# Optimization experiments

Hardware: AMD Instinct MI355X
Metric: run time of the kernel (lower is better)

Reference implementation:

```python
import jax, jax.numpy as jnp
import numpy as np
import math

FRACTION = 1.0 / math.e  # GOLDEN_ZONE_CENTER


def setup_inputs() -> dict:
    key = jax.random.key(0)
    x = jax.random.normal(key, (4, 4096, 2048), dtype=jnp.float32)
    return {"x": x}


def reference(x) -> jnp.ndarray:
    # Training-mode forward of BoltzmannGateSTE: keep only top-k (k = n/e)
    # activations by global magnitude, zero the rest.
    flat = jnp.abs(x).reshape(-1)
    n = flat.shape[0]
    k = max(1, int(n * FRACTION))  # static python int -> jit-friendly
    if k >= n:
        return x
    topk_vals, _ = jax.lax.top_k(flat, k)
    threshold = topk_vals[-1]  # k-th largest magnitude
    mask = (jnp.abs(x) >= threshold).astype(x.dtype)
    return x * mask
```

## Files before the change

### kernel.cpp

```cpp
#include <hip/hip_runtime.h>
#include <stdint.h>
#include <string.h>


#define SEL_T 1024

constexpr unsigned LO_BITS = 0x3F6147AEu;
constexpr unsigned HI_BITS = 0x3F6B851Fu;
constexpr unsigned NKEY    = HI_BITS - LO_BITS;
constexpr int      NCB     = (NKEY + 1023) / 1024;

constexpr int P_GRID = 4096;
constexpr int P_BLK  = 256;
constexpr int P_WPB  = P_BLK / 64;
constexpr int NWAVES = P_GRID * P_WPB;
constexpr int CAPW   = 128;

constexpr int NBIN1   = 4096;
constexpr int NFINE   = 1 << 19;
constexpr int NCOARSE = 512;
constexpr int F_GRID  = 256;
constexpr int F_BLK   = 256;

#define S_PREF 0
#define S_K1   1
#define S_T    2
#define S_FLAG 3

__device__ __forceinline__ bool gate_skip(const unsigned* state, int gate) {
    if (gate == 0) return false;
    unsigned fl = state[S_FLAG];
    return (gate == 1) ? (fl == 0u) : (fl != 0u);
}

__global__ __launch_bounds__(P_BLK, 8)
void pass_partition(const uint4* __restrict__ x, long long n4,
                    uint4* __restrict__ out, uint2* __restrict__ cand,
                    unsigned* __restrict__ wavecnt, unsigned* __restrict__ blkchi,
                    unsigned* __restrict__ fineH, unsigned* __restrict__ state)
{
    typedef unsigned uv4 __attribute__((ext_vector_type(4)));
    const int lane  = threadIdx.x & 63;
    const int wid   = threadIdx.x >> 6;
    const int gwave = blockIdx.x * P_WPB + wid;
    uint2* my = cand + (size_t)gwave * CAPW;
    const unsigned long long lt = (1ull << lane) - 1ull;

    unsigned wcnt = 0;
    unsigned chi  = 0;
    const long long stride = (long long)gridDim.x * P_BLK;
#pragma unroll 2
    for (long long i = (long long)blockIdx.x * P_BLK + threadIdx.x; i < n4; i += stride) {
        uint4 v = x[i];
        uint4 r;
        unsigned idx0 = (unsigned)(i << 2);
#define DO_COMP(c, off)                                                        \
        { unsigned b = v.c, u = b & 0x7FFFFFFFu;                               \
          bool kp = (u >= HI_BITS);                                            \
          bool cd = (u >= LO_BITS) & !kp;                                      \
          chi += (unsigned)kp;                                                 \
          r.c = kp ? b : 0u;                                                   \
          unsigned long long m = __ballot(cd);                                 \
          if (cd) {                                                            \
              atomicAdd(&fineH[u - LO_BITS], 1u);         \
              unsigned pos = wcnt + (unsigned)__popcll(m & lt);                \
              if (pos < (unsigned)CAPW) my[pos] = make_uint2(b, idx0 + off);   \
          }                                                                    \
          wcnt += (unsigned)__popcll(m); }
        DO_COMP(x, 0) DO_COMP(y, 1) DO_COMP(z, 2) DO_COMP(w, 3)
#undef DO_COMP
        __builtin_nontemporal_store(*(uv4*)&r, (uv4*)(out + i));
    }

    for (int m = 32; m; m >>= 1) chi += __shfl_xor(chi, m, 64);
    __shared__ unsigned s_chi[P_WPB];
    if (lane == 0) {
        s_chi[wid] = chi;
        wavecnt[gwave] = (wcnt < (unsigned)CAPW) ? wcnt : (unsigned)CAPW;
        if (wcnt > (unsigned)CAPW) atomicOr(&state[S_FLAG], 1u);
    }
    __syncthreads();
    if (threadIdx.x == 0) {
        unsigned a = 0;
        for (int w = 0; w < P_WPB; ++w) a += s_chi[w];
        blkchi[blockIdx.x] = a;
    }
}

__global__ __launch_bounds__(64)
void coarse_reduce(const unsigned* __restrict__ fineH, unsigned* __restrict__ coarseH)
{
    unsigned base = blockIdx.x << 10;
    unsigned s = 0;
    for (int t = threadIdx.x; t < 1024; t += 64) {
        unsigned key = base + t;
        s += (key < NKEY) ? fineH[key] : 0u;
    }
    for (int m = 32; m; m >>= 1) s += __shfl_xor(s, m, 64);
    if (threadIdx.x == 0) coarseH[blockIdx.x] = s;
}

__device__ void select_desc(const unsigned* __restrict__ hist, int nbins,
                            unsigned k, unsigned* s_scan, int* s_res)
{
    int tid = threadIdx.x;
    if (tid == 0) { s_res[0] = -1; s_res[1] = 0; }
    __syncthreads();
    unsigned running = 0;
    for (int top = nbins; top > 0; top -= SEL_T) {
        int bin = top - 1 - tid;
        unsigned v = (bin >= 0) ? hist[bin] : 0u;
        s_scan[tid] = v;
        __syncthreads();
        for (int off = 1; off < SEL_T; off <<= 1) {
            unsigned add = (tid >= off) ? s_scan[tid - off] : 0u;
            __syncthreads();
            s_scan[tid] += add;
            __syncthreads();
        }
        unsigned p     = s_scan[tid];
        unsigned pprev = (tid > 0) ? s_scan[tid - 1] : 0u;
        unsigned total = s_scan[SEL_T - 1];
        __syncthreads();
        if (running + total >= k) {
            if (bin >= 0 && running + p >= k && running + pprev < k) {
                s_res[0] = bin;
                s_res[1] = (int)(k - running - pprev);
            }
            __syncthreads();
            return;
        }
        running += total;
    }
    __syncthreads();
}

__global__ __launch_bounds__(SEL_T)
void fast_select(const unsigned* __restrict__ blkchi, const unsigned* __restrict__ wavecnt,
                 const unsigned* __restrict__ coarseH, const unsigned* __restrict__ fineH,
                 unsigned* __restrict__ state, unsigned k)
{
    if (state[S_FLAG]) return;
    __shared__ unsigned s_scan[SEL_T];
    __shared__ int s_res[2];
    __shared__ unsigned long long s_red[SEL_T / 64][2];
    __shared__ unsigned s_kp;
    __shared__ int s_bad;

    unsigned long long chi = 0, tot = 0;
    for (int i = threadIdx.x; i < P_GRID; i += SEL_T) chi += blkchi[i];
    for (int i = threadIdx.x; i < NWAVES; i += SEL_T) tot += wavecnt[i];
    for (int m = 32; m; m >>= 1) {
        chi += __shfl_xor(chi, m, 64);
        tot += __shfl_xor(tot, m, 64);
    }
    int wid = threadIdx.x >> 6, lane = threadIdx.x & 63;
    if (lane == 0) { s_red[wid][0] = chi; s_red[wid][1] = tot; }
    __syncthreads();
    if (threadIdx.x == 0) {
        unsigned long long C = 0, Tt = 0;
        for (int w = 0; w < SEL_T / 64; ++w) { C += s_red[w][0]; Tt += s_red[w][1]; }
        if (C >= (unsigned long long)k || C + Tt < (unsigned long long)k) {
            state[S_FLAG] = 1u;
            s_bad = 1;
        } else { s_bad = 0; s_kp = (unsigned)((unsigned long long)k - C); }
    }
    __syncthreads();
    if (s_bad) return;
    unsigned kp = s_kp;

    select_desc(coarseH, NCB, kp, s_scan, s_res);
    int cb      = s_res[0];
    unsigned r  = (unsigned)s_res[1];
    __syncthreads();
    int nfine = (int)NKEY - cb * 1024;
    if (nfine > 1024) nfine = 1024;
    select_desc(fineH + (size_t)cb * 1024, nfine, r, s_scan, s_res);
    int f = s_res[0];
    if (threadIdx.x == 0)
        state[S_T] = LO_BITS + (unsigned)(cb * 1024 + f);
}

__global__ __launch_bounds__(256)
void cand_fixup(const uint2* __restrict__ cand, const unsigned* __restrict__ state,
                float* __restrict__ out, long long n)
{
    if (state[S_FLAG]) return;
    unsigned T = state[S_T];
    long long total = (long long)NWAVES * CAPW;
    long long stride = (long long)gridDim.x * 256;
    for (long long j = (long long)blockIdx.x * 256 + threadIdx.x; j < total; j += stride) {
        uint2 e = cand[j];
        if ((e.x & 0x7FFFFFFFu) >= T && e.y < (unsigned long long)n)
            out[e.y] = __uint_as_float(e.x);
    }
}

__global__ __launch_bounds__(F_BLK)
void f_hist1(const uint4* __restrict__ x, long long n4, unsigned* __restrict__ histA,
             const unsigned* __restrict__ state, int gate)
{
    if (gate_skip(state, gate)) return;
    __shared__ unsigned h[NBIN1];
    for (int i = threadIdx.x; i < NBIN1; i += F_BLK) h[i] = 0u;
    __syncthreads();
    long long stride = (long long)gridDim.x * F_BLK;
    for (long long i = (long long)blockIdx.x * F_BLK + threadIdx.x; i < n4; i += stride) {
        uint4 v = x[i];
        atomicAdd(&h[(v.x & 0x7FFFFFFFu) >> 19], 1u);
        atomicAdd(&h[(v.y & 0x7FFFFFFFu) >> 19], 1u);
        atomicAdd(&h[(v.z & 0x7FFFFFFFu) >> 19], 1u);
        atomicAdd(&h[(v.w & 0x7FFFFFFFu) >> 19], 1u);
    }
    __syncthreads();
    for (int i = threadIdx.x; i < NBIN1; i += F_BLK)
        if (h[i]) atomicAdd(&histA[i], h[i]);
}

__global__ __launch_bounds__(SEL_T)
void f_select1(const unsigned* __restrict__ histA, unsigned* __restrict__ state,
               unsigned k, int gate)
{
    if (gate_skip(state, gate)) return;
    __shared__ unsigned s_scan[SEL_T];
    __shared__ int s_res[2];
    select_desc(histA, NBIN1, k, s_scan, s_res);
    if (threadIdx.x == 0) {
        state[S_PREF] = (s_res[0] < 0) ? 0u : (unsigned)s_res[0];
        state[S_K1]   = (s_res[0] < 0) ? 1u : (unsigned)s_res[1];
    }
}

__global__ __launch_bounds__(F_BLK)
void f_hist2(const uint4* __restrict__ x, long long n4, const unsigned* __restrict__ state,
             unsigned* __restrict__ fineB, unsigned* __restrict__ coarseB, int gate)
{
    if (gate_skip(state, gate)) return;
    __shared__ unsigned hc[NCOARSE];
    for (int i = threadIdx.x; i < NCOARSE; i += F_BLK) hc[i] = 0u;
    __syncthreads();
    unsigned pref = state[S_PREF];
    long long stride = (long long)gridDim.x * F_BLK;
    for (long long i = (long long)blockIdx.x * F_BLK + threadIdx.x; i < n4; i += stride) {
        uint4 v = x[i];
        unsigned u;
#define DO_C(c) u = v.c & 0x7FFFFFFFu;                                        \
        if ((u >> 19) == pref) {                                              \
            atomicAdd(&fineB[u & (NFINE - 1)], 1u);                           \
            atomicAdd(&hc[(u & (NFINE - 1)) >> 10], 1u); }
        DO_C(x) DO_C(y) DO_C(z) DO_C(w)
#undef DO_C
    }
    __syncthreads();
    for (int i = threadIdx.x; i < NCOARSE; i += F_BLK)
        if (hc[i]) atomicAdd(&coarseB[i], hc[i]);
}

__global__ __launch_bounds__(SEL_T)
void f_select2(const unsigned* __restrict__ fineB, const unsigned* __restrict__ coarseB,
               unsigned* __restrict__ state, int gate)
{
    if (gate_skip(state, gate)) return;
    __shared__ unsigned s_scan[SEL_T];
    __shared__ int s_res[2];
    unsigned pref = state[S_PREF];
    unsigned k    = state[S_K1];
    select_desc(coarseB, NCOARSE, k, s_scan, s_res);
    int c       = (s_res[0] < 0) ? 0 : s_res[0];
    unsigned k1 = (s_res[0] < 0) ? 1u : (unsigned)s_res[1];
    __syncthreads();
    select_desc(fineB + (size_t)c * 1024, 1024, k1, s_scan, s_res);
    int f = (s_res[0] < 0) ? 0 : s_res[0];
    if (threadIdx.x == 0)
        state[S_T] = (pref << 19) | ((unsigned)c << 10) | (unsigned)f;
}

__global__ __launch_bounds__(256)
void f_mask(const uint4* __restrict__ x, uint4* __restrict__ out, long long n4,
            const unsigned* __restrict__ state, int gate)
{
    if (gate_skip(state, gate)) return;
    unsigned t = state[S_T];
    long long stride = (long long)gridDim.x * 256;
    for (long long i = (long long)blockIdx.x * 256 + threadIdx.x; i < n4; i += stride) {
        uint4 v = x[i];
        uint4 r;
        r.x = ((v.x & 0x7FFFFFFFu) >= t) ? v.x : 0u;
        r.y = ((v.y & 0x7FFFFFFFu) >= t) ? v.y : 0u;
        r.z = ((v.z & 0x7FFFFFFFu) >= t) ? v.z : 0u;
        r.w = ((v.w & 0x7FFFFFFFu) >= t) ? v.w : 0u;
        out[i] = r;
    }
}

extern "C" void kernel_launch(void* const* d_in, const int* in_sizes, int n_in,
                              void* d_out, int out_size, void* d_ws, size_t ws_size,
                              hipStream_t stream)
{
    long long n = (long long)in_sizes[0];
    if (n <= 0) return;
    long long n4 = n >> 2;

    const double FRACTION = 1.0 / 2.718281828459045;
    long long k = (long long)((double)n * FRACTION);
    if (k < 1) k = 1;

    const size_t off_state   = 0;
    const size_t off_fineH   = 64;
    const size_t off_coarseH = off_fineH   + (((size_t)NKEY * 4 + 63) & ~63ull);
    const size_t off_fineB   = off_coarseH + (((size_t)NCB * 4 + 63) & ~63ull);
    const size_t off_coarseB = off_fineB   + (size_t)NFINE * 4;
    const size_t off_histA   = off_coarseB + (size_t)NCOARSE * 4;
    const size_t zero_end    = off_histA   + (size_t)NBIN1 * 4;
    const size_t off_wcnt    = zero_end;
    const size_t off_bchi    = off_wcnt + (size_t)NWAVES * 4;
    const size_t off_cand    = off_bchi + (size_t)P_GRID * 4;
    const size_t need_fast   = off_cand + (size_t)NWAVES * CAPW * 8;
    const size_t need_fb     = zero_end;

    uint8_t* base;
    unsigned* state = (unsigned*)d_ws;
    bool fast;
    if (ws_size >= need_fast)     { base = (uint8_t*)d_ws;  fast = true;  }
    else if (ws_size >= need_fb)  { base = (uint8_t*)d_ws;  fast = false; }
    else                          { base = (uint8_t*)d_out; fast = false;
                                    state = (unsigned*)d_ws; }

    unsigned* fineH   = (unsigned*)(base + off_fineH);
    unsigned* coarseH = (unsigned*)(base + off_coarseH);
    unsigned* fineB   = (unsigned*)(base + off_fineB);
    unsigned* coarseB = (unsigned*)(base + off_coarseB);
    unsigned* histA   = (unsigned*)(base + off_histA);
    unsigned* wavecnt = (unsigned*)(base + off_wcnt);
    unsigned* blkchi  = (unsigned*)(base + off_bchi);
    uint2*    cand    = (uint2*)   (base + off_cand);

    const uint4* x = (const uint4*)d_in[0];

    if (fast) {
        hipMemsetAsync(base, 0, zero_end, stream);
        pass_partition<<<P_GRID, P_BLK, 0, stream>>>(x, n4, (uint4*)d_out, cand,
                                                     wavecnt, blkchi, fineH, state);
        coarse_reduce <<<NCB, 64, 0, stream>>>(fineH, coarseH);
        fast_select   <<<1, SEL_T, 0, stream>>>(blkchi, wavecnt, coarseH, fineH,
                                                state, (unsigned)k);
        cand_fixup    <<<512, 256, 0, stream>>>(cand, state, (float*)d_out, n);
        f_hist1  <<<F_GRID, F_BLK, 0, stream>>>(x, n4, histA, state, 1);
        f_select1<<<1, SEL_T, 0, stream>>>(histA, state, (unsigned)k, 1);
        f_hist2  <<<F_GRID, F_BLK, 0, stream>>>(x, n4, state, fineB, coarseB, 1);
        f_select2<<<1, SEL_T, 0, stream>>>(fineB, coarseB, state, 1);
        f_mask   <<<1024, 256, 0, stream>>>(x, (uint4*)d_out, n4, state, 1);
    } else {
        if (state == (unsigned*)d_ws && base != (uint8_t*)d_ws)
            hipMemsetAsync(state, 0, 64, stream);
        hipMemsetAsync(base + off_fineB, 0,
                       ((size_t)NFINE + NCOARSE + NBIN1) * 4, stream);
        if (base == (uint8_t*)d_ws) hipMemsetAsync(state, 0, 64, stream);
        f_hist1  <<<F_GRID, F_BLK, 0, stream>>>(x, n4, histA, state, 0);
        f_select1<<<1, SEL_T, 0, stream>>>(histA, state, (unsigned)k, 0);
        f_hist2  <<<F_GRID, F_BLK, 0, stream>>>(x, n4, state, fineB, coarseB, 0);
        f_select2<<<1, SEL_T, 0, stream>>>(fineB, coarseB, state, 0);
        f_mask   <<<1024, 256, 0, stream>>>(x, (uint4*)d_out, n4, state, 0);
    }
}
```

Baseline: 307.2 us.

## Fuse coarse reduce into select via last-block pattern, ballot-count keeps

Merges the coarse histogram reduction and the single-block threshold select into one kernel. Each block reduces 1024 fine bins, and the last block to finish, detected with an atomic done counter, performs the selection, which removes one launch. The partition pass now counts kept elements with a ballot popcount instead of a per-thread sum plus a shuffle reduction. It also processes two explicit uint4 loads per iteration in place of the unroll pragma. The workspace layout is reordered to hold the done counter, and the select adds guards for a missing bin.

Measured after the change: 311.8 us. About the same (+1.5%).

```diff
diff --git a/kernel.cpp b/kernel.cpp
--- a/kernel.cpp
+++ b/kernel.cpp
@@ -47,35 +47,45 @@
     const unsigned long long lt = (1ull << lane) - 1ull;
 
     unsigned wcnt = 0;
-    unsigned chi  = 0;
-    const long long stride = (long long)gridDim.x * P_BLK;
-#pragma unroll 2
-    for (long long i = (long long)blockIdx.x * P_BLK + threadIdx.x; i < n4; i += stride) {
-        uint4 v = x[i];
-        uint4 r;
-        unsigned idx0 = (unsigned)(i << 2);
-#define DO_COMP(c, off)                                                        \
-        { unsigned b = v.c, u = b & 0x7FFFFFFFu;                               \
-          bool kp = (u >= HI_BITS);                                            \
-          bool cd = (u >= LO_BITS) & !kp;                                      \
-          chi += (unsigned)kp;                                                 \
-          r.c = kp ? b : 0u;                                                   \
-          unsigned long long m = __ballot(cd);                                 \
-          if (cd) {                                                            \
-              atomicAdd(&fineH[u - LO_BITS], 1u);         \
-              unsigned pos = wcnt + (unsigned)__popcll(m & lt);                \
-              if (pos < (unsigned)CAPW) my[pos] = make_uint2(b, idx0 + off);   \
-          }                                                                    \
-          wcnt += (unsigned)__popcll(m); }
-        DO_COMP(x, 0) DO_COMP(y, 1) DO_COMP(z, 2) DO_COMP(w, 3)
+    unsigned chiw = 0;
+
+#define DO_COMP(vv, rr, c, off, ibase)                                         \
+    { unsigned b = vv.c, u = b & 0x7FFFFFFFu;                                  \
+      unsigned long long mk = __ballot(u >= HI_BITS);                          \
+      unsigned long long mc = __ballot((u - LO_BITS) < NKEY);                  \
+      chiw += (unsigned)__popcll(mk);                                          \
+      rr.c = (u >= HI_BITS) ? b : 0u;                                          \
+      if ((u - LO_BITS) < NKEY) {                                              \
+          atomicAdd(&fineH[u - LO_BITS], 1u);             \
+          unsigned pos = wcnt + (unsigned)__popcll(mc & lt);                   \
+          if (pos < (unsigned)CAPW) my[pos] = make_uint2(b, (ibase) + off);    \
+      }                                                                        \
+      wcnt += (unsigned)__popcll(mc); }
+
+    const long long stride = (long long)gridDim.x * (P_BLK * 2);
+    for (long long i = (long long)blockIdx.x * (P_BLK * 2) + threadIdx.x; i < n4; i += stride) {
+        long long j = i + P_BLK;
+        bool h1 = (j < n4);
+        uint4 v0 = x[i];
+        uint4 v1;
+        if (h1) v1 = x[j];
+        uint4 r0, r1;
+        unsigned ib0 = (unsigned)(i << 2);
+        DO_COMP(v0, r0, x, 0, ib0) DO_COMP(v0, r0, y, 1, ib0)
+        DO_COMP(v0, r0, z, 2, ib0) DO_COMP(v0, r0, w, 3, ib0)
+        __builtin_nontemporal_store(*(uv4*)&r0, (uv4*)(out + i));
+        if (h1) {
+            unsigned ib1 = (unsigned)(j << 2);
+            DO_COMP(v1, r1, x, 0, ib1) DO_COMP(v1, r1, y, 1, ib1)
+            DO_COMP(v1, r1, z, 2, ib1) DO_COMP(v1, r1, w, 3, ib1)
+            __builtin_nontemporal_store(*(uv4*)&r1, (uv4*)(out + j));
+        }
+    }
 #undef DO_COMP
-        __builtin_nontemporal_store(*(uv4*)&r, (uv4*)(out + i));
-    }
-
-    for (int m = 32; m; m >>= 1) chi += __shfl_xor(chi, m, 64);
+
     __shared__ unsigned s_chi[P_WPB];
     if (lane == 0) {
-        s_chi[wid] = chi;
+        s_chi[wid] = chiw;
         wavecnt[gwave] = (wcnt < (unsigned)CAPW) ? wcnt : (unsigned)CAPW;
         if (wcnt > (unsigned)CAPW) atomicOr(&state[S_FLAG], 1u);
     }
@@ -85,19 +95,6 @@
         for (int w = 0; w < P_WPB; ++w) a += s_chi[w];
         blkchi[blockIdx.x] = a;
     }
-}
-
-__global__ __launch_bounds__(64)
-void coarse_reduce(const unsigned* __restrict__ fineH, unsigned* __restrict__ coarseH)
-{
-    unsigned base = blockIdx.x << 10;
-    unsigned s = 0;
-    for (int t = threadIdx.x; t < 1024; t += 64) {
-        unsigned key = base + t;
-        s += (key < NKEY) ? fineH[key] : 0u;
-    }
-    for (int m = 32; m; m >>= 1) s += __shfl_xor(s, m, 64);
-    if (threadIdx.x == 0) coarseH[blockIdx.x] = s;
 }
 
 __device__ void select_desc(const unsigned* __restrict__ hist, int nbins,
@@ -136,31 +133,48 @@
 }
 
 __global__ __launch_bounds__(SEL_T)
-void fast_select(const unsigned* __restrict__ blkchi, const unsigned* __restrict__ wavecnt,
-                 const unsigned* __restrict__ coarseH, const unsigned* __restrict__ fineH,
-                 unsigned* __restrict__ state, unsigned k)
-{
-    if (state[S_FLAG]) return;
+void reduce_select(const unsigned* __restrict__ fineH, unsigned* __restrict__ coarseH,
+                   const unsigned* __restrict__ blkchi, const unsigned* __restrict__ wavecnt,
+                   unsigned* __restrict__ state, unsigned* __restrict__ done_ctr,
+                   unsigned k)
+{
     __shared__ unsigned s_scan[SEL_T];
     __shared__ int s_res[2];
     __shared__ unsigned long long s_red[SEL_T / 64][2];
-    __shared__ unsigned s_kp;
+    __shared__ unsigned s_last, s_kp;
     __shared__ int s_bad;
 
+    int tid = threadIdx.x;
+    unsigned key = ((unsigned)blockIdx.x << 10) + (unsigned)tid;
+    unsigned s = (key < NKEY) ? fineH[key] : 0u;
+    for (int m = 32; m; m >>= 1) s += __shfl_xor(s, m, 64);
+    if ((tid & 63) == 0) s_red[tid >> 6][0] = s;
+    __syncthreads();
+    if (tid == 0) {
+        unsigned t = 0;
+        for (int w = 0; w < SEL_T / 64; ++w) t += (unsigned)s_red[w][0];
+        coarseH[blockIdx.x] = t;
+        __threadfence();
+        unsigned d = atomicAdd(done_ctr, 1u);
+        s_last = (d == (unsigned)(NCB - 1)) ? 1u : 0u;
+    }
+    __syncthreads();
+    if (!s_last) return;
+    __threadfence();
+
     unsigned long long chi = 0, tot = 0;
-    for (int i = threadIdx.x; i < P_GRID; i += SEL_T) chi += blkchi[i];
-    for (int i = threadIdx.x; i < NWAVES; i += SEL_T) tot += wavecnt[i];
+    for (int i = tid; i < P_GRID; i += SEL_T) chi += blkchi[i];
+    for (int i = tid; i < NWAVES; i += SEL_T) tot += wavecnt[i];
     for (int m = 32; m; m >>= 1) {
         chi += __shfl_xor(chi, m, 64);
         tot += __shfl_xor(tot, m, 64);
     }
-    int wid = threadIdx.x >> 6, lane = threadIdx.x & 63;
-    if (lane == 0) { s_red[wid][0] = chi; s_red[wid][1] = tot; }
-    __syncthreads();
-    if (threadIdx.x == 0) {
+    if ((tid & 63) == 0) { s_red[tid >> 6][0] = chi; s_red[tid >> 6][1] = tot; }
+    __syncthreads();
+    if (tid == 0) {
         unsigned long long C = 0, Tt = 0;
         for (int w = 0; w < SEL_T / 64; ++w) { C += s_red[w][0]; Tt += s_red[w][1]; }
-        if (C >= (unsigned long long)k || C + Tt < (unsigned long long)k) {
+        if (state[S_FLAG] || C >= (unsigned long long)k || C + Tt < (unsigned long long)k) {
             state[S_FLAG] = 1u;
             s_bad = 1;
         } else { s_bad = 0; s_kp = (unsigned)((unsigned long long)k - C); }
@@ -170,15 +184,17 @@
     unsigned kp = s_kp;
 
     select_desc(coarseH, NCB, kp, s_scan, s_res);
-    int cb      = s_res[0];
-    unsigned r  = (unsigned)s_res[1];
-    __syncthreads();
-    int nfine = (int)NKEY - cb * 1024;
-    if (nfine > 1024) nfine = 1024;
-    select_desc(fineH + (size_t)cb * 1024, nfine, r, s_scan, s_res);
-    int f = s_res[0];
-    if (threadIdx.x == 0)
-        state[S_T] = LO_BITS + (unsigned)(cb * 1024 + f);
+    int cb     = s_res[0];
+    unsigned r = (unsigned)s_res[1];
+    __syncthreads();
+    if (cb < 0) { if (tid == 0) state[S_FLAG] = 1u; return; }
+    int nf = (int)NKEY - (cb << 10);
+    if (nf > 1024) nf = 1024;
+    select_desc(fineH + ((size_t)cb << 10), nf, r, s_scan, s_res);
+    if (tid == 0) {
+        int f = (s_res[0] < 0) ? 0 : s_res[0];
+        state[S_T] = LO_BITS + (unsigned)((cb << 10) + f);
+    }
 }
 
 __global__ __launch_bounds__(256)
@@ -293,6 +309,8 @@
     }
 }
 
+static inline size_t align64(size_t v) { return (v + 63) & ~(size_t)63; }
+
 extern "C" void kernel_launch(void* const* d_in, const int* in_sizes, int n_in,
                               void* d_out, int out_size, void* d_ws, size_t ws_size,
                               hipStream_t stream)
@@ -305,10 +323,10 @@
     long long k = (long long)((double)n * FRACTION);
     if (k < 1) k = 1;
 
-    const size_t off_state   = 0;
-    const size_t off_fineH   = 64;
-    const size_t off_coarseH = off_fineH   + (((size_t)NKEY * 4 + 63) & ~63ull);
-    const size_t off_fineB   = off_coarseH + (((size_t)NCB * 4 + 63) & ~63ull);
+    const size_t off_done    = 64;
+    const size_t off_coarseH = 128;
+    const size_t off_fineH   = align64(off_coarseH + (size_t)NCB * 4);
+    const size_t off_fineB   = align64(off_fineH + (size_t)NKEY * 4);
     const size_t off_coarseB = off_fineB   + (size_t)NFINE * 4;
     const size_t off_histA   = off_coarseB + (size_t)NCOARSE * 4;
     const size_t zero_end    = off_histA   + (size_t)NBIN1 * 4;
@@ -323,11 +341,11 @@
     bool fast;
     if (ws_size >= need_fast)     { base = (uint8_t*)d_ws;  fast = true;  }
     else if (ws_size >= need_fb)  { base = (uint8_t*)d_ws;  fast = false; }
-    else                          { base = (uint8_t*)d_out; fast = false;
-                                    state = (unsigned*)d_ws; }
-
+    else                          { base = (uint8_t*)d_out; fast = false; }
+
+    unsigned* done_c  = (unsigned*)(base + off_done);
+    unsigned* coarseH = (unsigned*)(base + off_coarseH);
     unsigned* fineH   = (unsigned*)(base + off_fineH);
-    unsigned* coarseH = (unsigned*)(base + off_coarseH);
     unsigned* fineB   = (unsigned*)(base + off_fineB);
     unsigned* coarseB = (unsigned*)(base + off_coarseB);
     unsigned* histA   = (unsigned*)(base + off_histA);
@@ -341,9 +359,8 @@
         hipMemsetAsync(base, 0, zero_end, stream);
         pass_partition<<<P_GRID, P_BLK, 0, stream>>>(x, n4, (uint4*)d_out, cand,
                                                      wavecnt, blkchi, fineH, state);
-        coarse_reduce <<<NCB, 64, 0, stream>>>(fineH, coarseH);
-        fast_select   <<<1, SEL_T, 0, stream>>>(blkchi, wavecnt, coarseH, fineH,
-                                                state, (unsigned)k);
+        reduce_select <<<NCB, SEL_T, 0, stream>>>(fineH, coarseH, blkchi, wavecnt,
+                                                  state, done_c, (unsigned)k);
         cand_fixup    <<<512, 256, 0, stream>>>(cand, state, (float*)d_out, n);
         f_hist1  <<<F_GRID, F_BLK, 0, stream>>>(x, n4, histA, state, 1);
         f_select1<<<1, SEL_T, 0, stream>>>(histA, state, (unsigned)k, 1);
@@ -351,11 +368,10 @@
         f_select2<<<1, SEL_T, 0, stream>>>(fineB, coarseB, state, 1);
         f_mask   <<<1024, 256, 0, stream>>>(x, (uint4*)d_out, n4, state, 1);
     } else {
-        if (state == (unsigned*)d_ws && base != (uint8_t*)d_ws)
-            hipMemsetAsync(state, 0, 64, stream);
+        if (base != (uint8_t*)d_ws) hipMemsetAsync(state, 0, 64, stream);
+        else                        hipMemsetAsync(base, 0, 128, stream);
         hipMemsetAsync(base + off_fineB, 0,
                        ((size_t)NFINE + NCOARSE + NBIN1) * 4, stream);
-        if (base == (uint8_t*)d_ws) hipMemsetAsync(state, 0, 64, stream);
         f_hist1  <<<F_GRID, F_BLK, 0, stream>>>(x, n4, histA, state, 0);
         f_select1<<<1, SEL_T, 0, stream>>>(histA, state, (unsigned)k, 0);
         f_hist2  <<<F_GRID, F_BLK, 0, stream>>>(x, n4, state, fineB, coarseB, 0);
```
